# Kernel tuning notes

Measured on AMD Instinct MI355X. Metric: run time of the kernel, lower is better.

Reference implementation:

```python
import jax, jax.numpy as jnp
import numpy as np

N_NODES = 100000
N_EDGES = 800000


def gcn_conv(x, W, b, src, dst, ew, n):
    # PyG GCNConv with edge weights and self-loops already included in (src, dst, ew):
    # deg[i] = sum of incoming edge weights at i; norm_e = d^-1/2[src] * w_e * d^-1/2[dst]
    h = x @ W                                                  # [N, F_out]
    deg = jax.ops.segment_sum(ew, dst, num_segments=n)         # [N]
    dinv = jnp.where(deg > 0, jax.lax.rsqrt(deg), 0.0)
    norm = dinv[src] * ew * dinv[dst]                          # [E]
    out = jax.ops.segment_sum(h[src] * norm[:, None], dst, num_segments=n)
    return out + b


def add_self_loops(edge_index, edge_weight, n):
    loop = jnp.arange(n, dtype=edge_index.dtype)
    src = jnp.concatenate([edge_index[0], loop])
    dst = jnp.concatenate([edge_index[1], loop])
    ew = jnp.concatenate([edge_weight, jnp.ones((n,), edge_weight.dtype)])
    return src, dst, ew


def setup_inputs() -> dict:
    key = jax.random.key(0)
    ks = jax.random.split(key, 10)
    x = jax.random.normal(ks[0], (N_NODES, 5), jnp.float32)
    edge_index = jax.random.randint(ks[1], (2, N_EDGES), 0, N_NODES, dtype=jnp.int64)
    edge_weight = jax.random.uniform(ks[2], (N_EDGES,), jnp.float32)
    def glorot(k, fan_in, fan_out):
        s = float(np.sqrt(6.0 / (fan_in + fan_out)))
        return jax.random.uniform(k, (fan_in, fan_out), jnp.float32, -s, s)
    return {
        "x": x,
        "edge_index": edge_index,
        "edge_weight": edge_weight,
        "W1": glorot(ks[3], 5, 320),
        "b1": jnp.zeros((320,), jnp.float32),
        "W2": glorot(ks[4], 320, 160),
        "b2": jnp.zeros((160,), jnp.float32),
        "We": glorot(ks[5], 160, 80),
        "be": jnp.zeros((80,), jnp.float32),
    }


def reference(x, edge_index, edge_weight, W1, b1, W2, b2, We, be):
    n = x.shape[0]
    src, dst, ew = add_self_loops(edge_index, edge_weight, n)
    h = gcn_conv(x, W1, b1, src, dst, ew, n)        # conv1
    h = jax.nn.relu(h)
    h = gcn_conv(h, W2, b2, src, dst, ew, n)        # conv2
    return h @ We + be                              # embed linear
```

## Files before the change

kernel.cpp:

```cpp
#include <hip/hip_runtime.h>

#define NF0 5
#define F1 320
#define F2 160
#define F3 80

typedef float f32x4 __attribute__((ext_vector_type(4)));
typedef _Float16 f16x8 __attribute__((ext_vector_type(8)));


__global__ void k_binA(const void* ei, const float* __restrict__ ew, const int* __restrict__ flag,
                       int* __restrict__ bin_cnt , int2* __restrict__ bins,
                       int bin_stride, int* __restrict__ ovf_n, int* __restrict__ ovf,
                       int ovf_cap, int E) {
    int e = blockIdx.x * blockDim.x + threadIdx.x;
    if (e >= E) return;
    int s, d;
    if (*flag) {
        const long long* p = (const long long*)ei;
        s = (int)p[e]; d = (int)p[E + e];
    } else {
        const int* p = (const int*)ei;
        s = p[e]; d = p[E + e];
    }
    float w = ew[e];
    int b = d >> 8;
    int pos = atomicAdd(&bin_cnt[b * 16], 1);
    if (pos < bin_stride) {
        int2 pk;
        pk.x = s | ((d & 255) << 24);
        pk.y = __float_as_int(w);
        bins[(size_t)b * bin_stride + pos] = pk;
    } else {
        int o = atomicAdd(ovf_n, 1);
        if (o < ovf_cap) {
            ovf[3 * o] = s; ovf[3 * o + 1] = d; ovf[3 * o + 2] = __float_as_int(w);
        }
    }
}

__global__ void k_fixdeg(const int* __restrict__ ovf_n, const int* __restrict__ ovf, int ovf_cap,
                         float* __restrict__ deg) {
    int n = *ovf_n; if (n > ovf_cap) n = ovf_cap;
    for (int j = blockIdx.x * blockDim.x + threadIdx.x; j < n; j += gridDim.x * blockDim.x)
        atomicAdd(&deg[ovf[3 * j + 1]], __int_as_float(ovf[3 * j + 2]));
}


__global__ __launch_bounds__(256) void k_binB(const int2* __restrict__ bins, int bin_stride,
                                              const int* __restrict__ bin_cnt,
                                              float* __restrict__ deg ,
                                              int* __restrict__ cnt, int2* __restrict__ bucket,
                                              int cap, int* __restrict__ ovf_n,
                                              int* __restrict__ ovf, int ovf_cap, int N) {
    __shared__ float deg_l[256];
    __shared__ int cnt_l[256];
    int b = blockIdx.x, t = threadIdx.x;
    deg_l[t] = 0.f; cnt_l[t] = 0;
    __syncthreads();
    int ne = bin_cnt[b * 16]; if (ne > bin_stride) ne = bin_stride;
    const int2* bp = bins + (size_t)b * bin_stride;
    for (int j = t; j < ne; j += 256) {
        int2 pk = bp[j];
        int s = pk.x & 0xFFFFFF;
        int dl = ((unsigned int)pk.x) >> 24;
        atomicAdd(&deg_l[dl], __int_as_float(pk.y));
        int pos = atomicAdd(&cnt_l[dl], 1);
        int node = b * 256 + dl;
        if (pos < cap) {
            int2 out_pk; out_pk.x = s; out_pk.y = pk.y;
            bucket[(size_t)node * cap + pos] = out_pk;
        } else {
            int o = atomicAdd(ovf_n, 1);
            if (o < ovf_cap) { ovf[3 * o] = s; ovf[3 * o + 1] = node; ovf[3 * o + 2] = pk.y; }
        }
    }
    __syncthreads();
    int node = b * 256 + t;
    if (node < N) {
        float dsum = deg[node] + 1.0f + deg_l[t];
        deg[node] = rsqrtf(dsum);
        int c = cnt_l[t]; if (c > cap) c = cap;
        cnt[node] = c;
    }
}


__global__ void k_prep(const float* __restrict__ x, float* __restrict__ xp, int N, int padxB,
                       const float* __restrict__ W2, const float* __restrict__ We,
                       _Float16* __restrict__ Bh,
                       const float* __restrict__ b2, const float* __restrict__ be,
                       float* __restrict__ bc,
                       const unsigned int* __restrict__ ei32, int E, int* __restrict__ flag) {
    __shared__ int ok;
    int b = blockIdx.x;
    if (b < padxB) {
        int t = b * 256 + threadIdx.x;
        if (t < N * 8) {
            int f = t & 7, i = t >> 3;
            xp[t] = (f < NF0) ? x[i * NF0 + f] : 0.f;
        }
    } else if (b < padxB + 13) {
        int t = (b - padxB) * 256 + threadIdx.x;
        if (t >= 50 * 64) return;
        int fid = t >> 6, lane = t & 63;
        int kk = fid / 5, ct = fid % 5;
        int col = ct * 16 + (lane & 15);
        int row0 = kk * 32 + (lane >> 4) * 8;
        float acc[8] = {0.f, 0.f, 0.f, 0.f, 0.f, 0.f, 0.f, 0.f};
        for (int m = 0; m < F2; ++m) {
            float wv = We[m * F3 + col];
            #pragma unroll
            for (int i = 0; i < 8; ++i)
                acc[i] += W2[(size_t)(row0 + i) * F2 + m] * wv;
        }
        size_t ob = (size_t)t * 8;
        #pragma unroll
        for (int i = 0; i < 8; ++i)
            Bh[ob + i] = (_Float16)acc[i];
    } else if (b == padxB + 13) {
        int j = threadIdx.x;
        if (j < F3) {
            float s = be[j];
            for (int k = 0; k < F2; ++k) s += b2[k] * We[k * F3 + j];
            bc[j] = s;
        }
    } else {
        if (threadIdx.x == 0) ok = 1;
        __syncthreads();
        int npairs = E < 2048 ? E : 2048;
        for (int i = threadIdx.x; i < npairs; i += blockDim.x)
            if (ei32[2 * i + 1] != 0u) ok = 0;
        __syncthreads();
        if (threadIdx.x == 0) *flag = ok;
    }
}


__global__ void k_aggA(const float* __restrict__ xp, const float* __restrict__ dinv,
                       const int* __restrict__ cnt, int2* __restrict__ bucket, int cap,
                       float* __restrict__ agg1, int N) {
    int i = blockIdx.x * blockDim.x + threadIdx.x;
    if (i >= N) return;
    float di = dinv[i];
    float sc = di * di;
    float4 xv = *(const float4*)(xp + (size_t)i * 8);
    float x4 = xp[(size_t)i * 8 + 4];
    float a0 = xv.x * sc, a1 = xv.y * sc, a2 = xv.z * sc, a3 = xv.w * sc, a4 = x4 * sc;
    int c = cnt[i];
    int2* row = bucket + (size_t)i * cap;
    for (int j = 0; j < c; ++j) {
        int2 pk = row[j];
        int s = pk.x;
        float w = di * __int_as_float(pk.y) * dinv[s];
        row[j].y = __float_as_int(w);
        float4 sv = *(const float4*)(xp + (size_t)s * 8);
        float s4 = xp[(size_t)s * 8 + 4];
        a0 += sv.x * w; a1 += sv.y * w; a2 += sv.z * w; a3 += sv.w * w; a4 += s4 * w;
    }
    float* op = agg1 + (size_t)i * NF0;
    op[0] = a0; op[1] = a1; op[2] = a2; op[3] = a3; op[4] = a4;
}

__global__ void k_fixA(const float* __restrict__ x, const float* __restrict__ dinv,
                       const int* __restrict__ ovf_n, int* __restrict__ ovf, int ovf_cap,
                       float* __restrict__ agg1) {
    int n = *ovf_n; if (n > ovf_cap) n = ovf_cap;
    for (int j = blockIdx.x * blockDim.x + threadIdx.x; j < n; j += gridDim.x * blockDim.x) {
        int s = ovf[3 * j], d = ovf[3 * j + 1];
        float w = dinv[s] * __int_as_float(ovf[3 * j + 2]) * dinv[d];
        ovf[3 * j + 2] = __float_as_int(w);
        #pragma unroll
        for (int f = 0; f < NF0; ++f)
            atomicAdd(&agg1[(size_t)d * NF0 + f], x[(size_t)s * NF0 + f] * w);
    }
}


__global__ __launch_bounds__(256) void k_node(const float* __restrict__ agg1,
                                              const float* __restrict__ W1,
                                              const float* __restrict__ b1,
                                              const _Float16* __restrict__ Bh,
                                              _Float16* __restrict__ g, int N) {
    __shared__ float W_l[6 * F1];
    int tid = threadIdx.x;
    for (int i = tid; i < 480; i += 256) {
        float4 v = (i < 400) ? ((const float4*)W1)[i] : ((const float4*)b1)[i - 400];
        ((float4*)W_l)[i] = v;
    }
    __syncthreads();

    int w = tid >> 6, l = tid & 63;
    int nl = l & 15, kg = l >> 4;
    int base = blockIdx.x * 128 + w * 32;
    int n0 = base + nl, n1 = base + 16 + nl;

    float a0v[5] = {0.f, 0.f, 0.f, 0.f, 0.f};
    float a1v[5] = {0.f, 0.f, 0.f, 0.f, 0.f};
    if (n0 < N) {
        const float* ap = agg1 + (size_t)n0 * NF0;
        #pragma unroll
        for (int j = 0; j < 5; ++j) a0v[j] = ap[j];
    }
    if (n1 < N) {
        const float* ap = agg1 + (size_t)n1 * NF0;
        #pragma unroll
        for (int j = 0; j < 5; ++j) a1v[j] = ap[j];
    }

    f32x4 zero = {0.f, 0.f, 0.f, 0.f};
    f32x4 acc[10] = {zero, zero, zero, zero, zero, zero, zero, zero, zero, zero};
    const f16x8* bhp = (const f16x8*)Bh;

    #pragma unroll
    for (int kk = 0; kk < 10; ++kk) {
        int k0 = kk * 32 + kg * 8;
        float v0[8], v1[8];
        const float* bb = W_l + 5 * F1 + k0;
        #pragma unroll
        for (int i = 0; i < 8; ++i) { float b = bb[i]; v0[i] = b; v1[i] = b; }
        #pragma unroll
        for (int j = 0; j < 5; ++j) {
            const float* wp = W_l + j * F1 + k0;
            float aj0 = a0v[j], aj1 = a1v[j];
            #pragma unroll
            for (int i = 0; i < 8; ++i) {
                float wv = wp[i];
                v0[i] += aj0 * wv;
                v1[i] += aj1 * wv;
            }
        }
        f16x8 ah0, al0, ah1, al1;
        #pragma unroll
        for (int i = 0; i < 8; ++i) {
            float t0 = fmaxf(v0[i], 0.f);
            _Float16 h0 = (_Float16)t0;
            ah0[i] = h0;
            al0[i] = (_Float16)(t0 - (float)h0);
            float t1 = fmaxf(v1[i], 0.f);
            _Float16 h1 = (_Float16)t1;
            ah1[i] = h1;
            al1[i] = (_Float16)(t1 - (float)h1);
        }
        #pragma unroll
        for (int ct = 0; ct < 5; ++ct) {
            f16x8 bf = bhp[(kk * 5 + ct) * 64 + l];
            acc[ct] = __builtin_amdgcn_mfma_f32_16x16x32_f16(ah0, bf, acc[ct], 0, 0, 0);
            acc[ct] = __builtin_amdgcn_mfma_f32_16x16x32_f16(al0, bf, acc[ct], 0, 0, 0);
            acc[5 + ct] = __builtin_amdgcn_mfma_f32_16x16x32_f16(ah1, bf, acc[5 + ct], 0, 0, 0);
            acc[5 + ct] = __builtin_amdgcn_mfma_f32_16x16x32_f16(al1, bf, acc[5 + ct], 0, 0, 0);
        }
    }

    #pragma unroll
    for (int ct = 0; ct < 5; ++ct) {
        #pragma unroll
        for (int r = 0; r < 4; ++r) {
            int r0 = base + kg * 4 + r;
            if (r0 < N) g[(size_t)r0 * F3 + ct * 16 + nl] = (_Float16)acc[ct][r];
            int r1 = base + 16 + kg * 4 + r;
            if (r1 < N) g[(size_t)r1 * F3 + ct * 16 + nl] = (_Float16)acc[5 + ct][r];
        }
    }
}


__global__ __launch_bounds__(256) void k_aggB(const _Float16* __restrict__ g,
                                              const float* __restrict__ dinv,
                                              const float* __restrict__ bc,
                                              const int* __restrict__ cnt,
                                              const int2* __restrict__ bucket, int cap,
                                              float* __restrict__ out, int N) {
    int t = blockIdx.x * blockDim.x + threadIdx.x;
    if (t >= 5 * N) return;
    int i = t / 5;
    int c = (t - i * 5) << 4;
    float di = dinv[i];
    float sc = di * di;
    float acc[16];
    {
        const f16x8* sp = (const f16x8*)(g + (size_t)i * F3 + c);
        f16x8 u0 = sp[0], u1 = sp[1];
        const float4* bp = (const float4*)(bc + c);
        float4 q0 = bp[0], q1 = bp[1], q2 = bp[2], q3 = bp[3];
        acc[0]  = (float)u0[0] * sc + q0.x;  acc[1]  = (float)u0[1] * sc + q0.y;
        acc[2]  = (float)u0[2] * sc + q0.z;  acc[3]  = (float)u0[3] * sc + q0.w;
        acc[4]  = (float)u0[4] * sc + q1.x;  acc[5]  = (float)u0[5] * sc + q1.y;
        acc[6]  = (float)u0[6] * sc + q1.z;  acc[7]  = (float)u0[7] * sc + q1.w;
        acc[8]  = (float)u1[0] * sc + q2.x;  acc[9]  = (float)u1[1] * sc + q2.y;
        acc[10] = (float)u1[2] * sc + q2.z;  acc[11] = (float)u1[3] * sc + q2.w;
        acc[12] = (float)u1[4] * sc + q3.x;  acc[13] = (float)u1[5] * sc + q3.y;
        acc[14] = (float)u1[6] * sc + q3.z;  acc[15] = (float)u1[7] * sc + q3.w;
    }
    int cn = cnt[i];
    const int2* row = bucket + (size_t)i * cap;
    #pragma unroll 2
    for (int j = 0; j < cn; ++j) {
        int2 pk = row[j];
        float w = __int_as_float(pk.y);
        const f16x8* sp = (const f16x8*)(g + (size_t)pk.x * F3 + c);
        f16x8 a = sp[0], b8 = sp[1];
        #pragma unroll
        for (int e = 0; e < 8; ++e) {
            acc[e]     += (float)a[e]  * w;
            acc[8 + e] += (float)b8[e] * w;
        }
    }
    float4* op = (float4*)(out + (size_t)i * F3 + c);
    #pragma unroll
    for (int q = 0; q < 4; ++q) {
        float4 v;
        v.x = acc[q * 4 + 0]; v.y = acc[q * 4 + 1]; v.z = acc[q * 4 + 2]; v.w = acc[q * 4 + 3];
        op[q] = v;
    }
}

__global__ void k_fixB(const _Float16* __restrict__ g, const float* __restrict__ dinv,
                       const int* __restrict__ ovf_n, const int* __restrict__ ovf, int ovf_cap,
                       float* __restrict__ out) {
    int n = *ovf_n; if (n > ovf_cap) n = ovf_cap;
    for (int j = blockIdx.x * blockDim.x + threadIdx.x; j < n; j += gridDim.x * blockDim.x) {
        int s = ovf[3 * j], d = ovf[3 * j + 1];
        float w = __int_as_float(ovf[3 * j + 2]);
        for (int f = 0; f < F3; ++f)
            atomicAdd(&out[(size_t)d * F3 + f], (float)g[(size_t)s * F3 + f] * w);
    }
}


static inline size_t align256(size_t x) { return (x + 255) & ~(size_t)255; }

extern "C" void kernel_launch(void* const* d_in, const int* in_sizes, int n_in,
                              void* d_out, int out_size, void* d_ws, size_t ws_size,
                              hipStream_t stream) {
    const float* x  = (const float*)d_in[0];
    const void*  ei = d_in[1];
    const float* ew = (const float*)d_in[2];
    const float* W1 = (const float*)d_in[3];
    const float* b1 = (const float*)d_in[4];
    const float* W2 = (const float*)d_in[5];
    const float* b2 = (const float*)d_in[6];
    const float* We = (const float*)d_in[7];
    const float* be = (const float*)d_in[8];
    float* out = (float*)d_out;

    int N = in_sizes[0] / NF0;
    int E = in_sizes[2];

    const int OVF_CAP = 131072;
    const int BIN_STRIDE = 4096;
    int n_bins = (N + 255) >> 8;

    char* p = (char*)d_ws;
    auto alloc = [&](size_t bytes) { char* r = p; p += align256(bytes); return r; };
    int*   flag  = (int*)alloc(4);
    size_t zints = (size_t)N + 16 + (size_t)n_bins * 16;
    int*   zreg  = (int*)alloc(zints * 4);
    float* deg   = (float*)zreg;
    int*   ovf_n = zreg + N;
    int*   bin_cnt = zreg + N + 16;
    int*   cnt   = (int*)  alloc((size_t)N * 4);
    int*   ovf   = (int*)  alloc((size_t)OVF_CAP * 12);
    int2*  bins  = (int2*) alloc((size_t)n_bins * BIN_STRIDE * 8);
    float* xp    = (float*)alloc((size_t)N * 8 * 4);
    float* agg1  = (float*)alloc((size_t)N * NF0 * 4);
    float* bc    = (float*)alloc((size_t)F3 * 4);
    _Float16* Bh = (_Float16*)alloc((size_t)50 * 64 * 8 * 2);
    _Float16* g  = (_Float16*)alloc((size_t)N * F3 * 2);

    size_t used = (size_t)(p - (char*)d_ws);
    int cap = 24;
    if (ws_size > used) {
        size_t avail = (ws_size - used) / ((size_t)N * 8);
        if (avail < (size_t)cap) cap = (int)avail;
    } else cap = 4;
    if (cap < 4) cap = 4;
    int2* bucket = (int2*)alloc((size_t)N * cap * 8);

    int eb  = (E + 255) / 256;
    int nb1 = (N + 255) / 256;
    int padxB = (N * 8 + 255) / 256;

    hipMemsetAsync(zreg, 0, zints * 4, stream);
    k_prep<<<padxB + 15, 256, 0, stream>>>(x, xp, N, padxB, W2, We, Bh, b2, be, bc,
                                           (const unsigned int*)ei, E, flag);

    k_binA<<<eb, 256, 0, stream>>>(ei, ew, flag, bin_cnt, bins, BIN_STRIDE, ovf_n, ovf, OVF_CAP, E);
    k_fixdeg<<<16, 256, 0, stream>>>(ovf_n, ovf, OVF_CAP, deg);
    k_binB<<<n_bins, 256, 0, stream>>>(bins, BIN_STRIDE, bin_cnt, deg, cnt, bucket, cap,
                                       ovf_n, ovf, OVF_CAP, N);

    k_aggA<<<nb1, 256, 0, stream>>>(xp, deg, cnt, bucket, cap, agg1, N);
    k_fixA<<<16, 256, 0, stream>>>(x, deg, ovf_n, ovf, OVF_CAP, agg1);
    k_node<<<(N + 127) / 128, 256, 0, stream>>>(agg1, W1, b1, Bh, g, N);
    k_aggB<<<(5 * N + 255) / 256, 256, 0, stream>>>(g, deg, bc, cnt, bucket, cap, out, N);
    k_fixB<<<16, 256, 0, stream>>>(g, deg, ovf_n, ovf, OVF_CAP, out);
}
```

Measured before the change: 189.5 us.

## Split binning into degree pass and fused normalize-and-aggregate pass; halve k_node tile

Binning now runs in two passes. The first only accumulates degrees and writes dinv. The second re-reads the bins, computes the normalized edge weight, writes the bucket with weights already normalized, and accumulates the layer-1 aggregation in shared-memory atomics. This removes the separate k_aggA kernel and its re-read of the bucket array. k_node is also changed to process 16 rows per wave instead of 32, doubling the grid. The cost is a second pass over the bins, shared-memory float atomics, and less reuse of the B operand per wave in k_node.

```diff
diff --git a/kernel.cpp b/kernel.cpp
--- a/kernel.cpp
+++ b/kernel.cpp
@@ -47,41 +47,83 @@
 }
 
 
-__global__ __launch_bounds__(256) void k_binB(const int2* __restrict__ bins, int bin_stride,
-                                              const int* __restrict__ bin_cnt,
-                                              float* __restrict__ deg ,
-                                              int* __restrict__ cnt, int2* __restrict__ bucket,
-                                              int cap, int* __restrict__ ovf_n,
-                                              int* __restrict__ ovf, int ovf_cap, int N) {
+__global__ __launch_bounds__(256) void k_binB1(const int2* __restrict__ bins, int bin_stride,
+                                               const int* __restrict__ bin_cnt,
+                                               float* __restrict__ deg ,
+                                               int N) {
     __shared__ float deg_l[256];
+    int b = blockIdx.x, t = threadIdx.x;
+    deg_l[t] = 0.f;
+    __syncthreads();
+    int ne = bin_cnt[b * 16]; if (ne > bin_stride) ne = bin_stride;
+    const int2* bp = bins + (size_t)b * bin_stride;
+    for (int j = t; j < ne; j += 256) {
+        int2 pk = bp[j];
+        atomicAdd(&deg_l[((unsigned int)pk.x) >> 24], __int_as_float(pk.y));
+    }
+    __syncthreads();
+    int node = b * 256 + t;
+    if (node < N) deg[node] = rsqrtf(deg[node] + 1.0f + deg_l[t]);
+}
+
+
+__global__ __launch_bounds__(256) void k_binB2(const int2* __restrict__ bins, int bin_stride,
+                                               const int* __restrict__ bin_cnt,
+                                               const float* __restrict__ dinv,
+                                               const float* __restrict__ xp,
+                                               int* __restrict__ cnt, int2* __restrict__ bucket,
+                                               int cap, float* __restrict__ agg1,
+                                               int* __restrict__ ovf_n, int* __restrict__ ovf,
+                                               int ovf_cap, int N) {
     __shared__ int cnt_l[256];
+    __shared__ float dinv_l[256];
+    __shared__ float acc_l[256 * NF0];
     int b = blockIdx.x, t = threadIdx.x;
-    deg_l[t] = 0.f; cnt_l[t] = 0;
-    __syncthreads();
+    cnt_l[t] = 0;
+    int node0 = b * 256 + t;
+    dinv_l[t] = (node0 < N) ? dinv[node0] : 0.f;
+    for (int q = t; q < 256 * NF0; q += 256) acc_l[q] = 0.f;
+    __syncthreads();
+
     int ne = bin_cnt[b * 16]; if (ne > bin_stride) ne = bin_stride;
     const int2* bp = bins + (size_t)b * bin_stride;
     for (int j = t; j < ne; j += 256) {
         int2 pk = bp[j];
         int s = pk.x & 0xFFFFFF;
         int dl = ((unsigned int)pk.x) >> 24;
-        atomicAdd(&deg_l[dl], __int_as_float(pk.y));
+        float w = dinv[s] * __int_as_float(pk.y) * dinv_l[dl];
+        int node = b * 256 + dl;
         int pos = atomicAdd(&cnt_l[dl], 1);
-        int node = b * 256 + dl;
         if (pos < cap) {
-            int2 out_pk; out_pk.x = s; out_pk.y = pk.y;
+            int2 out_pk; out_pk.x = s; out_pk.y = __float_as_int(w);
             bucket[(size_t)node * cap + pos] = out_pk;
         } else {
             int o = atomicAdd(ovf_n, 1);
             if (o < ovf_cap) { ovf[3 * o] = s; ovf[3 * o + 1] = node; ovf[3 * o + 2] = pk.y; }
         }
-    }
-    __syncthreads();
-    int node = b * 256 + t;
-    if (node < N) {
-        float dsum = deg[node] + 1.0f + deg_l[t];
-        deg[node] = rsqrtf(dsum);
+        float4 sv = *(const float4*)(xp + (size_t)s * 8);
+        float s4 = xp[(size_t)s * 8 + 4];
+        atomicAdd(&acc_l[dl * NF0 + 0], sv.x * w);
+        atomicAdd(&acc_l[dl * NF0 + 1], sv.y * w);
+        atomicAdd(&acc_l[dl * NF0 + 2], sv.z * w);
+        atomicAdd(&acc_l[dl * NF0 + 3], sv.w * w);
+        atomicAdd(&acc_l[dl * NF0 + 4], s4 * w);
+    }
+    __syncthreads();
+
+    if (node0 < N) {
+        float di = dinv_l[t];
+        float sc = di * di;
+        float4 xv = *(const float4*)(xp + (size_t)node0 * 8);
+        float x4 = xp[(size_t)node0 * 8 + 4];
+        float* op = agg1 + (size_t)node0 * NF0;
+        op[0] = acc_l[t * NF0 + 0] + xv.x * sc;
+        op[1] = acc_l[t * NF0 + 1] + xv.y * sc;
+        op[2] = acc_l[t * NF0 + 2] + xv.z * sc;
+        op[3] = acc_l[t * NF0 + 3] + xv.w * sc;
+        op[4] = acc_l[t * NF0 + 4] + x4 * sc;
         int c = cnt_l[t]; if (c > cap) c = cap;
-        cnt[node] = c;
+        cnt[node0] = c;
     }
 }
 
@@ -136,32 +178,6 @@
     }
 }
 
-
-__global__ void k_aggA(const float* __restrict__ xp, const float* __restrict__ dinv,
-                       const int* __restrict__ cnt, int2* __restrict__ bucket, int cap,
-                       float* __restrict__ agg1, int N) {
-    int i = blockIdx.x * blockDim.x + threadIdx.x;
-    if (i >= N) return;
-    float di = dinv[i];
-    float sc = di * di;
-    float4 xv = *(const float4*)(xp + (size_t)i * 8);
-    float x4 = xp[(size_t)i * 8 + 4];
-    float a0 = xv.x * sc, a1 = xv.y * sc, a2 = xv.z * sc, a3 = xv.w * sc, a4 = x4 * sc;
-    int c = cnt[i];
-    int2* row = bucket + (size_t)i * cap;
-    for (int j = 0; j < c; ++j) {
-        int2 pk = row[j];
-        int s = pk.x;
-        float w = di * __int_as_float(pk.y) * dinv[s];
-        row[j].y = __float_as_int(w);
-        float4 sv = *(const float4*)(xp + (size_t)s * 8);
-        float s4 = xp[(size_t)s * 8 + 4];
-        a0 += sv.x * w; a1 += sv.y * w; a2 += sv.z * w; a3 += sv.w * w; a4 += s4 * w;
-    }
-    float* op = agg1 + (size_t)i * NF0;
-    op[0] = a0; op[1] = a1; op[2] = a2; op[3] = a3; op[4] = a4;
-}
-
 __global__ void k_fixA(const float* __restrict__ x, const float* __restrict__ dinv,
                        const int* __restrict__ ovf_n, int* __restrict__ ovf, int ovf_cap,
                        float* __restrict__ agg1) {
@@ -192,63 +208,47 @@
 
     int w = tid >> 6, l = tid & 63;
     int nl = l & 15, kg = l >> 4;
-    int base = blockIdx.x * 128 + w * 32;
-    int n0 = base + nl, n1 = base + 16 + nl;
+    int base = blockIdx.x * 64 + w * 16;
+    int n0 = base + nl;
 
     float a0v[5] = {0.f, 0.f, 0.f, 0.f, 0.f};
-    float a1v[5] = {0.f, 0.f, 0.f, 0.f, 0.f};
     if (n0 < N) {
         const float* ap = agg1 + (size_t)n0 * NF0;
         #pragma unroll
         for (int j = 0; j < 5; ++j) a0v[j] = ap[j];
     }
-    if (n1 < N) {
-        const float* ap = agg1 + (size_t)n1 * NF0;
-        #pragma unroll
-        for (int j = 0; j < 5; ++j) a1v[j] = ap[j];
-    }
 
     f32x4 zero = {0.f, 0.f, 0.f, 0.f};
-    f32x4 acc[10] = {zero, zero, zero, zero, zero, zero, zero, zero, zero, zero};
+    f32x4 acc[5] = {zero, zero, zero, zero, zero};
     const f16x8* bhp = (const f16x8*)Bh;
 
     #pragma unroll
     for (int kk = 0; kk < 10; ++kk) {
         int k0 = kk * 32 + kg * 8;
-        float v0[8], v1[8];
+        float v0[8];
         const float* bb = W_l + 5 * F1 + k0;
         #pragma unroll
-        for (int i = 0; i < 8; ++i) { float b = bb[i]; v0[i] = b; v1[i] = b; }
+        for (int i = 0; i < 8; ++i) v0[i] = bb[i];
         #pragma unroll
         for (int j = 0; j < 5; ++j) {
             const float* wp = W_l + j * F1 + k0;
-            float aj0 = a0v[j], aj1 = a1v[j];
+            float aj0 = a0v[j];
             #pragma unroll
-            for (int i = 0; i < 8; ++i) {
-                float wv = wp[i];
-                v0[i] += aj0 * wv;
-                v1[i] += aj1 * wv;
-            }
-        }
-        f16x8 ah0, al0, ah1, al1;
+            for (int i = 0; i < 8; ++i) v0[i] += aj0 * wp[i];
+        }
+        f16x8 ah0, al0;
         #pragma unroll
         for (int i = 0; i < 8; ++i) {
             float t0 = fmaxf(v0[i], 0.f);
             _Float16 h0 = (_Float16)t0;
             ah0[i] = h0;
             al0[i] = (_Float16)(t0 - (float)h0);
-            float t1 = fmaxf(v1[i], 0.f);
-            _Float16 h1 = (_Float16)t1;
-            ah1[i] = h1;
-            al1[i] = (_Float16)(t1 - (float)h1);
         }
         #pragma unroll
         for (int ct = 0; ct < 5; ++ct) {
             f16x8 bf = bhp[(kk * 5 + ct) * 64 + l];
             acc[ct] = __builtin_amdgcn_mfma_f32_16x16x32_f16(ah0, bf, acc[ct], 0, 0, 0);
             acc[ct] = __builtin_amdgcn_mfma_f32_16x16x32_f16(al0, bf, acc[ct], 0, 0, 0);
-            acc[5 + ct] = __builtin_amdgcn_mfma_f32_16x16x32_f16(ah1, bf, acc[5 + ct], 0, 0, 0);
-            acc[5 + ct] = __builtin_amdgcn_mfma_f32_16x16x32_f16(al1, bf, acc[5 + ct], 0, 0, 0);
         }
     }
 
@@ -258,8 +258,6 @@
         for (int r = 0; r < 4; ++r) {
             int r0 = base + kg * 4 + r;
             if (r0 < N) g[(size_t)r0 * F3 + ct * 16 + nl] = (_Float16)acc[ct][r];
-            int r1 = base + 16 + kg * 4 + r;
-            if (r1 < N) g[(size_t)r1 * F3 + ct * 16 + nl] = (_Float16)acc[5 + ct][r];
         }
     }
 }
@@ -378,7 +376,6 @@
     int2* bucket = (int2*)alloc((size_t)N * cap * 8);
 
     int eb  = (E + 255) / 256;
-    int nb1 = (N + 255) / 256;
     int padxB = (N * 8 + 255) / 256;
 
     hipMemsetAsync(zreg, 0, zints * 4, stream);
@@ -387,12 +384,12 @@
 
     k_binA<<<eb, 256, 0, stream>>>(ei, ew, flag, bin_cnt, bins, BIN_STRIDE, ovf_n, ovf, OVF_CAP, E);
     k_fixdeg<<<16, 256, 0, stream>>>(ovf_n, ovf, OVF_CAP, deg);
-    k_binB<<<n_bins, 256, 0, stream>>>(bins, BIN_STRIDE, bin_cnt, deg, cnt, bucket, cap,
-                                       ovf_n, ovf, OVF_CAP, N);
-
-    k_aggA<<<nb1, 256, 0, stream>>>(xp, deg, cnt, bucket, cap, agg1, N);
+    k_binB1<<<n_bins, 256, 0, stream>>>(bins, BIN_STRIDE, bin_cnt, deg, N);
+    k_binB2<<<n_bins, 256, 0, stream>>>(bins, BIN_STRIDE, bin_cnt, deg, xp, cnt, bucket, cap,
+                                        agg1, ovf_n, ovf, OVF_CAP, N);
     k_fixA<<<16, 256, 0, stream>>>(x, deg, ovf_n, ovf, OVF_CAP, agg1);
-    k_node<<<(N + 127) / 128, 256, 0, stream>>>(agg1, W1, b1, Bh, g, N);
+
+    k_node<<<(N + 63) / 64, 256, 0, stream>>>(agg1, W1, b1, Bh, g, N);
     k_aggB<<<(5 * N + 255) / 256, 256, 0, stream>>>(g, deg, bc, cnt, bucket, cap, out, N);
     k_fixB<<<16, 256, 0, stream>>>(g, deg, ovf_n, ovf, OVF_CAP, out);
 }
```

Result: no change. 189.3 us (-0.1%).
